# Kernel tuning notes

Hardware: AMD Instinct MI355X
Metric: run time of the kernel (lower is better)

## Reference

```python
import jax, jax.numpy as jnp
import numpy as np


def _mlp(x, w1, b1, w2, b2):
    # torch Mlp: fc1 -> GELU (exact erf) -> fc2, dropout off in eval
    h = jax.nn.gelu(x @ w1 + b1, approximate=False)
    return h @ w2 + b2


def _nearest(x, oh, ow):
    # torch F.interpolate mode='nearest' on [B,h,w,d]: src = floor(dst*in/out)
    h, w = x.shape[1], x.shape[2]
    ih = (np.arange(oh) * h) // oh
    iw = (np.arange(ow) * w) // ow
    return x[:, ih][:, :, iw]


def setup_inputs() -> dict:
    key = jax.random.key(0)
    ks = jax.random.split(key, 8)
    B, s0, dim, nPnt, new2 = 4, 12, 256, 128, 48  # new_size=24
    sc = 0.02
    return {
        "token_init": jax.random.normal(ks[0], (B, s0, s0, dim), jnp.float32),
        "point_token": jax.random.normal(ks[1], (B, nPnt, dim), jnp.float32),
        "nr_w1": jax.random.normal(ks[2], (nPnt, 4 * nPnt), jnp.float32) * sc,
        "nr_b1": jnp.zeros((4 * nPnt,), jnp.float32),
        "nr_w2": jax.random.normal(ks[3], (4 * nPnt, nPnt), jnp.float32) * sc,
        "nr_b2": jnp.zeros((nPnt,), jnp.float32),
        "na_w1": jax.random.normal(ks[4], (nPnt, 4 * nPnt), jnp.float32) * sc,
        "na_b1": jnp.zeros((4 * nPnt,), jnp.float32),
        "na_w2": jax.random.normal(ks[5], (4 * nPnt, nPnt), jnp.float32) * sc,
        "na_b2": jnp.zeros((nPnt,), jnp.float32),
        "tf_w1": jax.random.normal(ks[6], (new2, new2), jnp.float32) * sc,
        "tf_b1": jnp.zeros((new2,), jnp.float32),
        "tf_w2": jax.random.normal(ks[7], (new2, 1), jnp.float32) * sc,
        "tf_b2": jnp.zeros((1,), jnp.float32),
        "height": 120,
        "width": 160,
    }


def reference(token_init, point_token, nr_w1, nr_b1, nr_w2, nr_b2,
              na_w1, na_b1, na_w2, na_b2, tf_w1, tf_b1, tf_w2, tf_b2,
              height, width):
    B, nPnt, dim = point_token.shape
    new_size = tf_w1.shape[0] // 2
    scale = dim ** (-0.5)
    # is_init=False path: repeat_interleave x2 along H and W
    t = jnp.repeat(jnp.repeat(token_init, 2, axis=1), 2, axis=2)  # [B,2s,2s,d]
    token_raw = _nearest(t, height, width)                        # [B,H,W,d]
    t_exp = _nearest(t, new_size, new_size)                       # [B,sH,sW,d]
    sH = sW = new_size
    token_templ = t_exp.reshape(B, sH * sW, dim)
    node_adj = jnp.einsum('bnd,bpd->bnp', token_templ, point_token) * scale
    node_adj = _mlp(node_adj, nr_w1, nr_b1, nr_w2, nr_b2)
    node_adj = node_adj.reshape(B, sH, sW, nPnt)
    node_w = jnp.einsum('bhwp,bhwd->bhpd', node_adj, t_exp) * (sW ** -0.5)
    node_h = jnp.einsum('bhwp,bhwd->bwpd', node_adj, t_exp) * (sH ** -0.5)
    token_n = jnp.concatenate([node_w, node_h], axis=1)           # [B,2s,nPnt,d]
    x = token_n.reshape(B, sH + sW, nPnt * dim).transpose(0, 2, 1)  # [B,nPnt*d,2s]
    token_fused = _mlp(x, tf_w1, tf_b1, tf_w2, tf_b2)             # [B,nPnt*d,1]
    token_fused = token_fused.reshape(B, nPnt, dim)
    token_raw_f = token_raw.reshape(B, height * width, dim)
    node_attn = jnp.einsum('bnd,bpd->bnp', token_raw_f, point_token) * scale
    node_attn = jax.nn.softmax(_mlp(node_attn, na_w1, na_b1, na_w2, na_b2), axis=-1)
    token_new = node_attn @ token_fused + token_raw_f             # [B,HW,d]
    return token_new
```

## Files before the change

### kernel.cpp

```cpp
#include <hip/hip_runtime.h>
#include <math.h>

#define B     4
#define DIM   256
#define NP    128
#define NS    144
#define HID   512
#define NROW  576
#define H_OUT 120
#define W_OUT 160

__device__ __forceinline__ float gelu_exact(float x) {
    return 0.5f * x * (1.0f + erff(x * 0.70710678118654752440f));
}

__global__ __launch_bounds__(256) void k_mlp(
    const float* __restrict__ ti, const float* __restrict__ pt,
    const float* __restrict__ nr_w1, const float* __restrict__ nr_b1,
    const float* __restrict__ nr_w2, const float* __restrict__ nr_b2,
    const float* __restrict__ na_w1, const float* __restrict__ na_b1,
    const float* __restrict__ na_w2, const float* __restrict__ na_b2,
    float* __restrict__ nadjT, float* __restrict__ attn)
{
    const int mlp  = blockIdx.x / 144;
    const int tile = blockIdx.x % 144;
    const int g0 = tile * 4;
    const int b  = g0 / NS;
    const int n0 = g0 % NS;
    const int t  = threadIdx.x;

    const float* __restrict__ w1 = mlp ? na_w1 : nr_w1;
    const float* __restrict__ b1 = mlp ? na_b1 : nr_b1;
    const float* __restrict__ w2 = mlp ? na_w2 : nr_w2;
    const float* __restrict__ b2 = mlp ? na_b2 : nr_b2;

    __shared__ float4 xs4[4][64];
    __shared__ float  qs[4][NP];
    __shared__ float  hs[4][HID];
    __shared__ float  par[8][4][NP];
    __shared__ float  red[4][NP];

    {
        const int r = t >> 6, c = t & 63;
        xs4[r][c] = ((const float4*)ti)[(size_t)(g0 + r) * 64 + c];
    }
    __syncthreads();

    const int p  = t & 127;
    const int rh = t >> 7;
    {
        const float4* __restrict__ pr =
            (const float4*)pt + (size_t)(b * NP + p) * 64;
        float a0 = 0.f, a1 = 0.f;
        #pragma unroll 8
        for (int i = 0; i < 64; ++i) {
            const float4 v  = pr[i];
            const float4 x0 = xs4[rh][i];
            const float4 x1 = xs4[rh + 2][i];
            a0 += v.x*x0.x + v.y*x0.y + v.z*x0.z + v.w*x0.w;
            a1 += v.x*x1.x + v.y*x1.y + v.z*x1.z + v.w*x1.w;
        }
        qs[rh][p]     = a0 * 0.0625f;
        qs[rh + 2][p] = a1 * 0.0625f;
    }
    __syncthreads();

    {
        const int kq = t & 127;
        const int k0 = kq * 4;
        float4 acc0 = *(const float4*)(b1 + k0);
        float4 acc1 = acc0;
        const float* __restrict__ wp = w1 + k0;
        #pragma unroll 8
        for (int pp = 0; pp < NP; ++pp) {
            const float4 w4 = *(const float4*)(wp + (size_t)pp * HID);
            const float q0 = qs[rh][pp];
            const float q1 = qs[rh + 2][pp];
            acc0.x += q0*w4.x; acc0.y += q0*w4.y;
            acc0.z += q0*w4.z; acc0.w += q0*w4.w;
            acc1.x += q1*w4.x; acc1.y += q1*w4.y;
            acc1.z += q1*w4.z; acc1.w += q1*w4.w;
        }
        float4 o0, o1;
        o0.x = gelu_exact(acc0.x); o0.y = gelu_exact(acc0.y);
        o0.z = gelu_exact(acc0.z); o0.w = gelu_exact(acc0.w);
        o1.x = gelu_exact(acc1.x); o1.y = gelu_exact(acc1.y);
        o1.z = gelu_exact(acc1.z); o1.w = gelu_exact(acc1.w);
        ((float4*)hs[rh])[kq]     = o0;
        ((float4*)hs[rh + 2])[kq] = o1;
    }
    __syncthreads();

    {
        const int pq = t & 31;
        const int p0 = pq * 4;
        const int kg = t >> 5;
        float4 a0 = make_float4(0.f,0.f,0.f,0.f);
        float4 a1 = a0, a2 = a0, a3 = a0;
        const float4* __restrict__ w24 = (const float4*)(w2 + p0);
        #pragma unroll 8
        for (int i = 0; i < 64; ++i) {
            const int k = kg * 64 + i;
            const float4 w4 = w24[(size_t)k * 32];
            const float h0 = hs[0][k], h1 = hs[1][k];
            const float h2 = hs[2][k], h3 = hs[3][k];
            a0.x += h0*w4.x; a0.y += h0*w4.y; a0.z += h0*w4.z; a0.w += h0*w4.w;
            a1.x += h1*w4.x; a1.y += h1*w4.y; a1.z += h1*w4.z; a1.w += h1*w4.w;
            a2.x += h2*w4.x; a2.y += h2*w4.y; a2.z += h2*w4.z; a2.w += h2*w4.w;
            a3.x += h3*w4.x; a3.y += h3*w4.y; a3.z += h3*w4.z; a3.w += h3*w4.w;
        }
        ((float4*)par[kg][0])[pq] = a0;
        ((float4*)par[kg][1])[pq] = a1;
        ((float4*)par[kg][2])[pq] = a2;
        ((float4*)par[kg][3])[pq] = a3;
    }
    __syncthreads();

    float lg0 = b2[p], lg1 = lg0;
    #pragma unroll
    for (int kg = 0; kg < 8; ++kg) {
        lg0 += par[kg][rh][p];
        lg1 += par[kg][rh + 2][p];
    }

    if (mlp == 0) {
        float* __restrict__ dst = nadjT + (size_t)(b * NP + p) * NS + n0;
        dst[rh]     = lg0;
        dst[rh + 2] = lg1;
    } else {
        red[rh][p] = lg0; red[rh + 2][p] = lg1;
        __syncthreads();
        for (int s = 64; s > 0; s >>= 1) {
            if (p < s) {
                red[rh][p]     = fmaxf(red[rh][p],     red[rh][p + s]);
                red[rh + 2][p] = fmaxf(red[rh + 2][p], red[rh + 2][p + s]);
            }
            __syncthreads();
        }
        const float m0 = red[rh][0], m1 = red[rh + 2][0];
        __syncthreads();
        const float e0 = expf(lg0 - m0), e1 = expf(lg1 - m1);
        red[rh][p] = e0; red[rh + 2][p] = e1;
        __syncthreads();
        for (int s = 64; s > 0; s >>= 1) {
            if (p < s) {
                red[rh][p]     += red[rh][p + s];
                red[rh + 2][p] += red[rh + 2][p + s];
            }
            __syncthreads();
        }
        attn[(size_t)(g0 + rh) * NP + p]     = e0 / red[rh][0];
        attn[(size_t)(g0 + rh + 2) * NP + p] = e1 / red[rh + 2][0];
    }
}

__global__ __launch_bounds__(256) void k_fold(
    const float* __restrict__ nadjT, const float* __restrict__ ti,
    const float* __restrict__ w1, const float* __restrict__ b1,
    const float* __restrict__ w2, const float* __restrict__ b2,
    float* __restrict__ tf)
{
    const int b = blockIdx.x >> 7;
    const int p = blockIdx.x & 127;
    const int t = threadIdx.x;
    __shared__ float an[NS];
    __shared__ float w1p[24][48];
    __shared__ float b1s[48];
    __shared__ float w2s[48];

    if (t < 36) {
        ((float4*)an)[t] =
            ((const float4*)(nadjT + (size_t)(b * NP + p) * NS))[t];
    }
    if (t >= 192 && t < 240) {
        const int k = t - 192;
        b1s[k] = b1[k];
        w2s[k] = w2[k];
    }
    for (int i = t; i < 24 * 48; i += 256) {
        const int m = i / 48, k = i - m * 48;
        w1p[m][k] = w1[(2 * m) * 48 + k] + w1[(2 * m + 1) * 48 + k];
    }
    __syncthreads();

    const int d = t;
    const float* __restrict__ tb = ti + (size_t)b * NS * DIM + d;
    float v[24];
    #pragma unroll
    for (int m = 0; m < 24; ++m) v[m] = 0.f;
    #pragma unroll
    for (int y = 0; y < 12; ++y) {
        #pragma unroll
        for (int x = 0; x < 12; ++x) {
            const int n = y * 12 + x;
            const float tv = tb[n * DIM];
            const float a  = an[n];
            v[y]      += a * tv;
            v[12 + x] += a * tv;
        }
    }
    const float c = 0.40824829046386301637f;
    #pragma unroll
    for (int m = 0; m < 24; ++m) v[m] *= c;

    float acc = b2[0];
    for (int k = 0; k < 48; ++k) {
        float tt = b1s[k];
        #pragma unroll
        for (int m = 0; m < 24; ++m) tt += v[m] * w1p[m][k];
        acc += gelu_exact(tt) * w2s[k];
    }
    tf[(size_t)(b * NP + p) * DIM + d] = acc;
}

__global__ __launch_bounds__(256) void k_final(
    const float* __restrict__ attn, const float* __restrict__ tf,
    const float* __restrict__ ti, float4* __restrict__ out)
{
    const int g = blockIdx.x;
    const int b = g / NS;
    const int n = g % NS;
    const int t = threadIdx.x;
    const int dq = t & 63;
    const int pg = t >> 6;

    __shared__ float  at[NP];
    __shared__ float4 par4[4][64];
    __shared__ float4 rowf[64];

    if (t < NP) at[t] = attn[(size_t)g * NP + t];
    __syncthreads();

    const float4* __restrict__ tp = (const float4*)tf + (size_t)b * NP * 64 + dq;
    float4 acc = make_float4(0.f, 0.f, 0.f, 0.f);
    #pragma unroll 8
    for (int i = 0; i < 32; ++i) {
        const int pp = pg * 32 + i;
        const float  a  = at[pp];
        const float4 tv = tp[(size_t)pp * 64];
        acc.x += a * tv.x; acc.y += a * tv.y;
        acc.z += a * tv.z; acc.w += a * tv.w;
    }
    par4[pg][dq] = acc;
    __syncthreads();

    if (t < 64) {
        float4 s = par4[0][t];
        const float4 s1 = par4[1][t], s2 = par4[2][t], s3 = par4[3][t];
        const float4 tiv = ((const float4*)ti)[(size_t)g * 64 + t];
        s.x += s1.x + s2.x + s3.x + tiv.x;
        s.y += s1.y + s2.y + s3.y + tiv.y;
        s.z += s1.z + s2.z + s3.z + tiv.z;
        s.w += s1.w + s2.w + s3.w + tiv.w;
        rowf[t] = s;
    }
    __syncthreads();

    const int y = n / 12, x = n % 12;
    const int w_lo = (40 * x + 2) / 3;
    const int w_hi = (40 * x + 42) / 3;
    const float4 val = rowf[dq];
    for (int h = 10 * y; h < 10 * y + 10; ++h) {
        float4* __restrict__ orow = out + (size_t)((b * H_OUT + h) * W_OUT) * 64 + dq;
        for (int w = w_lo + pg; w < w_hi; w += 4) {
            orow[(size_t)w * 64] = val;
        }
    }
}

extern "C" void kernel_launch(void* const* d_in, const int* in_sizes, int n_in,
                              void* d_out, int out_size, void* d_ws, size_t ws_size,
                              hipStream_t stream) {
    (void)in_sizes; (void)n_in; (void)out_size; (void)ws_size;
    const float* token_init  = (const float*)d_in[0];
    const float* point_token = (const float*)d_in[1];
    const float* nr_w1 = (const float*)d_in[2];
    const float* nr_b1 = (const float*)d_in[3];
    const float* nr_w2 = (const float*)d_in[4];
    const float* nr_b2 = (const float*)d_in[5];
    const float* na_w1 = (const float*)d_in[6];
    const float* na_b1 = (const float*)d_in[7];
    const float* na_w2 = (const float*)d_in[8];
    const float* na_b2 = (const float*)d_in[9];
    const float* tf_w1 = (const float*)d_in[10];
    const float* tf_b1 = (const float*)d_in[11];
    const float* tf_w2 = (const float*)d_in[12];
    const float* tf_b2 = (const float*)d_in[13];

    float* out = (float*)d_out;
    float* ws  = (float*)d_ws;
    float* nadjT = ws;
    float* attn  = nadjT + NROW * NP;
    float* tf    = attn + NROW * NP;

    k_mlp<<<288, 256, 0, stream>>>(token_init, point_token,
                                   nr_w1, nr_b1, nr_w2, nr_b2,
                                   na_w1, na_b1, na_w2, na_b2,
                                   nadjT, attn);
    k_fold<<<B * NP, 256, 0, stream>>>(nadjT, token_init,
                                       tf_w1, tf_b1, tf_w2, tf_b2, tf);
    k_final<<<NROW, 256, 0, stream>>>(attn, tf, token_init, (float4*)out);
}
```

Measured before the change: 171.1 us.

## Stage point tokens in LDS for QK dot and split final broadcast across blocks

In k_mlp, the first dot product now stages point_token in 32-row chunks into padded shared memory (a union reused later for the MLP buffers), so each thread reads LDS instead of a strided global row, and the 256-wide reduction is split into two halves. k_final is launched with twice as many blocks, each writing half of the 10 output rows, to spread the large output store over more workgroups. A launch-bounds occupancy hint is added. The trade-off is redundant attn·tf computation per half-block and extra syncs in the chunked staging loop.

```diff
diff --git a/kernel.cpp b/kernel.cpp
--- a/kernel.cpp
+++ b/kernel.cpp
@@ -14,7 +14,7 @@
     return 0.5f * x * (1.0f + erff(x * 0.70710678118654752440f));
 }
 
-__global__ __launch_bounds__(256) void k_mlp(
+__global__ __launch_bounds__(256, 2) void k_mlp(
     const float* __restrict__ ti, const float* __restrict__ pt,
     const float* __restrict__ nr_w1, const float* __restrict__ nr_b1,
     const float* __restrict__ nr_w2, const float* __restrict__ nr_b2,
@@ -34,35 +34,53 @@
     const float* __restrict__ w2 = mlp ? na_w2 : nr_w2;
     const float* __restrict__ b2 = mlp ? na_b2 : nr_b2;
 
-    __shared__ float4 xs4[4][64];
-    __shared__ float  qs[4][NP];
-    __shared__ float  hs[4][HID];
-    __shared__ float  par[8][4][NP];
-    __shared__ float  red[4][NP];
+    __shared__ float xs[4][DIM];
+    __shared__ float parA[2][4][NP];
+    __shared__ float qs[4][NP];
+    union BU {
+        float pts[32][DIM + 1];
+        struct {
+            float hs[4][HID];
+            float par[8][4][NP];
+            float red[4][NP];
+        } bc;
+    };
+    __shared__ BU u;
 
     {
         const int r = t >> 6, c = t & 63;
-        xs4[r][c] = ((const float4*)ti)[(size_t)(g0 + r) * 64 + c];
-    }
-    __syncthreads();
+        ((float4*)xs[r])[c] = ((const float4*)ti)[(size_t)(g0 + r) * 64 + c];
+    }
+
+    const int p_l = t & 31;
+    const int rr  = (t >> 5) & 3;
+    const int dh  = t >> 7;
+    for (int chunk = 0; chunk < 4; ++chunk) {
+        const int p0 = chunk * 32;
+        const float4* __restrict__ src =
+            (const float4*)pt + (size_t)(b * NP + p0) * 64;
+        #pragma unroll
+        for (int i = t; i < 32 * 64; i += 256) {
+            const int row = i >> 6, c4 = i & 63;
+            const float4 v = src[(size_t)row * 64 + c4];
+            float* __restrict__ dst = &u.pts[row][c4 * 4];
+            dst[0] = v.x; dst[1] = v.y; dst[2] = v.z; dst[3] = v.w;
+        }
+        __syncthreads();
+        float acc = 0.f;
+        #pragma unroll 8
+        for (int d2 = 0; d2 < 128; ++d2) {
+            const int d = dh * 128 + d2;
+            acc += xs[rr][d] * u.pts[p_l][d];
+        }
+        parA[dh][rr][p0 + p_l] = acc;
+        __syncthreads();
+    }
 
     const int p  = t & 127;
     const int rh = t >> 7;
-    {
-        const float4* __restrict__ pr =
-            (const float4*)pt + (size_t)(b * NP + p) * 64;
-        float a0 = 0.f, a1 = 0.f;
-        #pragma unroll 8
-        for (int i = 0; i < 64; ++i) {
-            const float4 v  = pr[i];
-            const float4 x0 = xs4[rh][i];
-            const float4 x1 = xs4[rh + 2][i];
-            a0 += v.x*x0.x + v.y*x0.y + v.z*x0.z + v.w*x0.w;
-            a1 += v.x*x1.x + v.y*x1.y + v.z*x1.z + v.w*x1.w;
-        }
-        qs[rh][p]     = a0 * 0.0625f;
-        qs[rh + 2][p] = a1 * 0.0625f;
-    }
+    qs[rh][p]     = (parA[0][rh][p]     + parA[1][rh][p])     * 0.0625f;
+    qs[rh + 2][p] = (parA[0][rh + 2][p] + parA[1][rh + 2][p]) * 0.0625f;
     __syncthreads();
 
     {
@@ -86,8 +104,8 @@
         o0.z = gelu_exact(acc0.z); o0.w = gelu_exact(acc0.w);
         o1.x = gelu_exact(acc1.x); o1.y = gelu_exact(acc1.y);
         o1.z = gelu_exact(acc1.z); o1.w = gelu_exact(acc1.w);
-        ((float4*)hs[rh])[kq]     = o0;
-        ((float4*)hs[rh + 2])[kq] = o1;
+        ((float4*)u.bc.hs[rh])[kq]     = o0;
+        ((float4*)u.bc.hs[rh + 2])[kq] = o1;
     }
     __syncthreads();
 
@@ -102,25 +120,25 @@
         for (int i = 0; i < 64; ++i) {
             const int k = kg * 64 + i;
             const float4 w4 = w24[(size_t)k * 32];
-            const float h0 = hs[0][k], h1 = hs[1][k];
-            const float h2 = hs[2][k], h3 = hs[3][k];
+            const float h0 = u.bc.hs[0][k], h1 = u.bc.hs[1][k];
+            const float h2 = u.bc.hs[2][k], h3 = u.bc.hs[3][k];
             a0.x += h0*w4.x; a0.y += h0*w4.y; a0.z += h0*w4.z; a0.w += h0*w4.w;
             a1.x += h1*w4.x; a1.y += h1*w4.y; a1.z += h1*w4.z; a1.w += h1*w4.w;
             a2.x += h2*w4.x; a2.y += h2*w4.y; a2.z += h2*w4.z; a2.w += h2*w4.w;
             a3.x += h3*w4.x; a3.y += h3*w4.y; a3.z += h3*w4.z; a3.w += h3*w4.w;
         }
-        ((float4*)par[kg][0])[pq] = a0;
-        ((float4*)par[kg][1])[pq] = a1;
-        ((float4*)par[kg][2])[pq] = a2;
-        ((float4*)par[kg][3])[pq] = a3;
+        ((float4*)u.bc.par[kg][0])[pq] = a0;
+        ((float4*)u.bc.par[kg][1])[pq] = a1;
+        ((float4*)u.bc.par[kg][2])[pq] = a2;
+        ((float4*)u.bc.par[kg][3])[pq] = a3;
     }
     __syncthreads();
 
     float lg0 = b2[p], lg1 = lg0;
     #pragma unroll
     for (int kg = 0; kg < 8; ++kg) {
-        lg0 += par[kg][rh][p];
-        lg1 += par[kg][rh + 2][p];
+        lg0 += u.bc.par[kg][rh][p];
+        lg1 += u.bc.par[kg][rh + 2][p];
     }
 
     if (mlp == 0) {
@@ -128,29 +146,31 @@
         dst[rh]     = lg0;
         dst[rh + 2] = lg1;
     } else {
-        red[rh][p] = lg0; red[rh + 2][p] = lg1;
+        u.bc.red[rh][p] = lg0; u.bc.red[rh + 2][p] = lg1;
         __syncthreads();
         for (int s = 64; s > 0; s >>= 1) {
             if (p < s) {
-                red[rh][p]     = fmaxf(red[rh][p],     red[rh][p + s]);
-                red[rh + 2][p] = fmaxf(red[rh + 2][p], red[rh + 2][p + s]);
+                u.bc.red[rh][p] =
+                    fmaxf(u.bc.red[rh][p], u.bc.red[rh][p + s]);
+                u.bc.red[rh + 2][p] =
+                    fmaxf(u.bc.red[rh + 2][p], u.bc.red[rh + 2][p + s]);
             }
             __syncthreads();
         }
-        const float m0 = red[rh][0], m1 = red[rh + 2][0];
+        const float m0 = u.bc.red[rh][0], m1 = u.bc.red[rh + 2][0];
         __syncthreads();
         const float e0 = expf(lg0 - m0), e1 = expf(lg1 - m1);
-        red[rh][p] = e0; red[rh + 2][p] = e1;
+        u.bc.red[rh][p] = e0; u.bc.red[rh + 2][p] = e1;
         __syncthreads();
         for (int s = 64; s > 0; s >>= 1) {
             if (p < s) {
-                red[rh][p]     += red[rh][p + s];
-                red[rh + 2][p] += red[rh + 2][p + s];
+                u.bc.red[rh][p]     += u.bc.red[rh][p + s];
+                u.bc.red[rh + 2][p] += u.bc.red[rh + 2][p + s];
             }
             __syncthreads();
         }
-        attn[(size_t)(g0 + rh) * NP + p]     = e0 / red[rh][0];
-        attn[(size_t)(g0 + rh + 2) * NP + p] = e1 / red[rh + 2][0];
+        attn[(size_t)(g0 + rh) * NP + p]     = e0 / u.bc.red[rh][0];
+        attn[(size_t)(g0 + rh + 2) * NP + p] = e1 / u.bc.red[rh + 2][0];
     }
 }
 
@@ -217,7 +237,8 @@
     const float* __restrict__ attn, const float* __restrict__ tf,
     const float* __restrict__ ti, float4* __restrict__ out)
 {
-    const int g = blockIdx.x;
+    const int g    = blockIdx.x >> 1;
+    const int half = blockIdx.x & 1;
     const int b = g / NS;
     const int n = g % NS;
     const int t = threadIdx.x;
@@ -260,7 +281,8 @@
     const int w_lo = (40 * x + 2) / 3;
     const int w_hi = (40 * x + 42) / 3;
     const float4 val = rowf[dq];
-    for (int h = 10 * y; h < 10 * y + 10; ++h) {
+    const int h0 = 10 * y + 5 * half;
+    for (int h = h0; h < h0 + 5; ++h) {
         float4* __restrict__ orow = out + (size_t)((b * H_OUT + h) * W_OUT) * 64 + dq;
         for (int w = w_lo + pg; w < w_hi; w += 4) {
             orow[(size_t)w * 64] = val;
@@ -299,5 +321,5 @@
                                    nadjT, attn);
     k_fold<<<B * NP, 256, 0, stream>>>(nadjT, token_init,
                                        tf_w1, tf_b1, tf_w2, tf_b2, tf);
-    k_final<<<NROW, 256, 0, stream>>>(attn, tf, token_init, (float4*)out);
-}
+    k_final<<<NROW * 2, 256, 0, stream>>>(attn, tf, token_init, (float4*)out);
+}
```

Result: no change. 168.2 us (-1.7%).
